# Optimization experiments

Hardware: AMD Instinct MI355X
Metric: run time of the kernel (lower is better)

The kernel has to match this reference:

```python
import jax, jax.numpy as jnp
import numpy as np
import math

EPS = 1e-08
A_CONST = 0.14855178144710912
B_CONST = -0.35487039130661086


def _sdpa(q, k, v):
    # q,k,v: [..., n, d]
    d = q.shape[-1]
    scores = jnp.einsum('...nd,...md->...nm', q / math.sqrt(d), k)
    attn = jax.nn.softmax(scores, axis=-1)
    return jnp.einsum('...nm,...md->...nd', attn, v)


def _lln_attention(q, k, v):
    # global std-based rescaling (torch .std() uses ddof=1), no grad through sigmas
    sig_q = jax.lax.stop_gradient(jnp.std(q, ddof=1))
    sig_k = jax.lax.stop_gradient(jnp.std(k, ddof=1))
    sig_tild = ((sig_q ** 2 * sig_k ** 2 - B_CONST) / (2.0 * A_CONST)) ** 0.5
    alpha = sig_tild / sig_q
    beta = sig_tild / sig_k
    q = alpha * q
    k = beta * k
    q = q - jnp.max(q, axis=-1, keepdims=True)
    k = k - jnp.max(k, axis=(-2, -1), keepdims=True)
    Q = jnp.exp(q)  # [B,H,N,D]
    K = jnp.exp(k)
    # non-causal (mask=None) path
    S = jnp.einsum('bhnd,bhd->bhn', Q, K.sum(axis=-2)) + EPS
    KV = jnp.einsum('bhnd,bhne->bhde', K, v)  # [B,H,D,D]
    out = jnp.einsum('bhnd,bhde->bhne', Q, KV) / S[..., None]
    return out


def _block_diag_attention(q, k, v):
    B, H, N, D = q.shape
    ND = D * (N // D)
    h = H * (ND // D)
    Qb = q[:, :, :ND, :].reshape(B, h, D, D)
    Kb = k[:, :, :ND, :].reshape(B, h, D, D)
    Vb = v[:, :, :ND, :].reshape(B, h, D, D)
    out_blocks = _sdpa(Qb, Kb, Vb).reshape(B, H, ND, D)
    if ND < N:
        out_rem = _sdpa(q[:, :, ND:, :], k[:, :, ND:, :], v[:, :, ND:, :])
        return jnp.concatenate([out_blocks, out_rem], axis=-2)
    return out_blocks


def setup_inputs() -> dict:
    key = jax.random.key(0)
    kq, kk, kv = jax.random.split(key, 3)
    shape = (4, 16, 4096, 64)
    return {
        'q': jax.random.normal(kq, shape, dtype=jnp.float32),
        'k': jax.random.normal(kk, shape, dtype=jnp.float32),
        'v': jax.random.normal(kv, shape, dtype=jnp.float32),
    }


def reference(q, k, v):
    lin = _lln_attention(q, k, v)
    diag = _block_diag_attention(q, k, v)
    return 0.5 * (lin + diag)
```

## Files before the change

### kernel.cpp

```cpp
#include <hip/hip_runtime.h>
#include <math.h>

#define SEQ    4096
#define DIM    64
#define NHEADS 64
#define ELEMS  (NHEADS * SEQ * DIM)

typedef __attribute__((ext_vector_type(8))) short short8;
typedef __attribute__((ext_vector_type(4))) float f32x4;

#define MFMA16(a, b, c) __builtin_amdgcn_mfma_f32_16x16x32_bf16((a), (b), (c), 0, 0, 0)

__device__ __forceinline__ short f2b(float f) {
    union { float f; unsigned u; } x; x.f = f;
    return (short)((x.u + 0x7FFFu + ((x.u >> 16) & 1u)) >> 16);
}

__global__ __launch_bounds__(256) void reduce_stats(const float* __restrict__ q,
                                                    const float* __restrict__ kk,
                                                    float* __restrict__ ws) {
    int bid = blockIdx.x;
    int t = threadIdx.x;
    int isk = bid >> 10;
    int b = bid & 1023;
    const float4* x4 = (const float4*)((isk ? kk : q) + (long)b * 16384);
    float s = 0.f, sq = 0.f, mx = -1e30f;
#pragma unroll
    for (int it = 0; it < 16; ++it) {
        float4 v = x4[it * 256 + t];
        s += v.x + v.y + v.z + v.w;
        sq += v.x * v.x + v.y * v.y + v.z * v.z + v.w * v.w;
        mx = fmaxf(mx, fmaxf(fmaxf(v.x, v.y), fmaxf(v.z, v.w)));
    }
#pragma unroll
    for (int m = 32; m > 0; m >>= 1) {
        s += __shfl_xor(s, m);
        sq += __shfl_xor(sq, m);
        mx = fmaxf(mx, __shfl_xor(mx, m));
    }
    __shared__ float ls[4], lsq[4], lm[4];
    int w = t >> 6, lane = t & 63;
    if (lane == 0) { ls[w] = s; lsq[w] = sq; lm[w] = mx; }
    __syncthreads();
    if (t == 0) {
        float S = 0.f, SQ = 0.f, M = -1e30f;
        for (int i = 0; i < 4; ++i) { S += ls[i]; SQ += lsq[i]; M = fmaxf(M, lm[i]); }
        ws[isk * 2048 + b] = S;
        ws[isk * 2048 + 1024 + b] = SQ;
        if (isk) ws[4096 + b] = M;
    }
}

__global__ __launch_bounds__(256) void compute_params(float* __restrict__ ws) {
    const float* pqs = ws;
    const float* pqq = ws + 1024;
    const float* pks = ws + 2048;
    const float* pkq = ws + 3072;
    const float* pkm = ws + 4096;
    float* params = ws + 5120;
    int t = threadIdx.x;
    float qs = 0.f, qq = 0.f, ks = 0.f, kq = 0.f;
    for (int i = t; i < 1024; i += 256) {
        qs += pqs[i]; qq += pqq[i]; ks += pks[i]; kq += pkq[i];
    }
#pragma unroll
    for (int m = 32; m > 0; m >>= 1) {
        qs += __shfl_xor(qs, m); qq += __shfl_xor(qq, m);
        ks += __shfl_xor(ks, m); kq += __shfl_xor(kq, m);
    }
    __shared__ float l[4][4];
    __shared__ float lab[2];
    int w = t >> 6, lane = t & 63;
    if (lane == 0) { l[w][0] = qs; l[w][1] = qq; l[w][2] = ks; l[w][3] = kq; }
    __syncthreads();
    if (t == 0) {
        float QS = 0.f, QQ = 0.f, KS = 0.f, KQ = 0.f;
        for (int i = 0; i < 4; ++i) { QS += l[i][0]; QQ += l[i][1]; KS += l[i][2]; KQ += l[i][3]; }
        const double M = (double)ELEMS;
        double varq = ((double)QQ - (double)QS * (double)QS / M) / (M - 1.0);
        double vark = ((double)KQ - (double)KS * (double)KS / M) / (M - 1.0);
        const double A = 0.14855178144710912;
        const double B = -0.35487039130661086;
        double st2 = (varq * vark - B) / (2.0 * A);
        float alpha = (float)sqrt(st2 / varq);
        float beta  = (float)sqrt(st2 / vark);
        params[0] = alpha; params[1] = beta;
        lab[0] = alpha; lab[1] = beta;
    }
    __syncthreads();
    if (t < 64) {
        float m = -1e30f;
        for (int i = 0; i < 16; ++i) m = fmaxf(m, pkm[t * 16 + i]);
        params[2 + t] = lab[1] * m;
    }
}

__global__ __launch_bounds__(256, 4) void kv_kernel(const float* __restrict__ k,
                                                    const float* __restrict__ v,
                                                    const float* __restrict__ params,
                                                    float* __restrict__ Ksum,
                                                    float* __restrict__ KVt) {
    __shared__ short kt[64][40];
    __shared__ short vt[64][40];
    int t = threadIdx.x;
    int head = blockIdx.x >> 4, part = blockIdx.x & 15;
    float beta = params[1], kms = params[2 + head];
    int rp = t & 15, cg = t >> 4;
    int w = t >> 6, lane = t & 63;
    int am = lane & 15, ak8 = (lane >> 4) * 8;
    long rowbase = (long)head * SEQ + part * 256;
    f32x4 acc[4];
#pragma unroll
    for (int i = 0; i < 4; ++i) acc[i] = (f32x4)0.f;
    float ksc[4] = {0.f, 0.f, 0.f, 0.f};
    for (int ch = 0; ch < 8; ++ch) {
        long r0 = rowbase + ch * 32 + rp * 2;
        const float* kp = k + r0 * DIM + cg * 4;
        const float* vp = v + r0 * DIM + cg * 4;
        float4 ka = *(const float4*)kp;
        float4 kb2 = *(const float4*)(kp + DIM);
        float4 va = *(const float4*)vp;
        float4 vb2 = *(const float4*)(vp + DIM);
        float ea[4] = {__expf(beta * ka.x - kms), __expf(beta * ka.y - kms),
                       __expf(beta * ka.z - kms), __expf(beta * ka.w - kms)};
        float eb[4] = {__expf(beta * kb2.x - kms), __expf(beta * kb2.y - kms),
                       __expf(beta * kb2.z - kms), __expf(beta * kb2.w - kms)};
        float va_[4] = {va.x, va.y, va.z, va.w};
        float vb_[4] = {vb2.x, vb2.y, vb2.z, vb2.w};
        if (ch) __syncthreads();
#pragma unroll
        for (int j = 0; j < 4; ++j) {
            ksc[j] += ea[j] + eb[j];
            unsigned pk = (unsigned)(unsigned short)f2b(ea[j]) |
                          ((unsigned)(unsigned short)f2b(eb[j]) << 16);
            *(unsigned*)&kt[cg * 4 + j][rp * 2] = pk;
            unsigned pv = (unsigned)(unsigned short)f2b(va_[j]) |
                          ((unsigned)(unsigned short)f2b(vb_[j]) << 16);
            *(unsigned*)&vt[cg * 4 + j][rp * 2] = pv;
        }
        __syncthreads();
        short8 af = *(const short8*)&kt[w * 16 + am][ak8];
#pragma unroll
        for (int nt = 0; nt < 4; ++nt) {
            short8 bf = *(const short8*)&vt[nt * 16 + am][ak8];
            acc[nt] = MFMA16(af, bf, acc[nt]);
        }
    }
    float* KVh = KVt + head * 4096;
#pragma unroll
    for (int nt = 0; nt < 4; ++nt)
#pragma unroll
        for (int r = 0; r < 4; ++r) {
            int d = w * 16 + (lane >> 4) * 4 + r;
            int e = nt * 16 + am;
            atomicAdd(&KVh[e * 64 + d], acc[nt][r]);
        }
#pragma unroll
    for (int m = 1; m < 16; m <<= 1)
#pragma unroll
        for (int j = 0; j < 4; ++j) ksc[j] += __shfl_xor(ksc[j], m);
    if (rp == 0) {
#pragma unroll
        for (int j = 0; j < 4; ++j) atomicAdd(&Ksum[head * 64 + cg * 4 + j], ksc[j]);
    }
}

__global__ __launch_bounds__(256, 4) void fused_kernel(const float* __restrict__ q,
                                                       const float* __restrict__ k,
                                                       const float* __restrict__ v,
                                                       const float* __restrict__ params,
                                                       const float* __restrict__ Ksum,
                                                       const float* __restrict__ KVt,
                                                       float* __restrict__ out) {
    constexpr int LD = 72;
    __shared__ short qb[64][LD];
    __shared__ short kb[64][LD];
    __shared__ short vtb[64][LD];
    __shared__ short kvb[64][LD];
    __shared__ float lksum[64];
    __shared__ float lqmax[64];
    __shared__ float lsinv[64];

    int t = threadIdx.x;
    int head = blockIdx.x >> 6, rb = blockIdx.x & 63;
    long base = ((long)head * SEQ + rb * 64) * DIM;
    float alpha = params[0];
    int w = t >> 6, lane = t & 63;
    int am = lane & 15, ak8 = (lane >> 4) * 8;

    float4 qraw[4];
#pragma unroll
    for (int it = 0; it < 4; ++it) {
        int idx = it * 256 + t;
        int r = idx >> 4, c4 = idx & 15;
        float4 qv = *(const float4*)(q + base + r * DIM + c4 * 4);
        float4 kv2 = *(const float4*)(k + base + r * DIM + c4 * 4);
        float4 kvv = *(const float4*)(KVt + head * 4096 + r * DIM + c4 * 4);
        qraw[it] = qv;
        *(unsigned*)&qb[r][c4 * 4] = (unsigned)(unsigned short)f2b(qv.x) | ((unsigned)(unsigned short)f2b(qv.y) << 16);
        *(unsigned*)&qb[r][c4 * 4 + 2] = (unsigned)(unsigned short)f2b(qv.z) | ((unsigned)(unsigned short)f2b(qv.w) << 16);
        *(unsigned*)&kb[r][c4 * 4] = (unsigned)(unsigned short)f2b(kv2.x) | ((unsigned)(unsigned short)f2b(kv2.y) << 16);
        *(unsigned*)&kb[r][c4 * 4 + 2] = (unsigned)(unsigned short)f2b(kv2.z) | ((unsigned)(unsigned short)f2b(kv2.w) << 16);
        *(unsigned*)&kvb[r][c4 * 4] = (unsigned)(unsigned short)f2b(kvv.x) | ((unsigned)(unsigned short)f2b(kvv.y) << 16);
        *(unsigned*)&kvb[r][c4 * 4 + 2] = (unsigned)(unsigned short)f2b(kvv.z) | ((unsigned)(unsigned short)f2b(kvv.w) << 16);
        float m = fmaxf(fmaxf(qv.x, qv.y), fmaxf(qv.z, qv.w));
#pragma unroll
        for (int msk = 8; msk >= 1; msk >>= 1) m = fmaxf(m, __shfl_xor(m, msk));
        if (c4 == 0) lqmax[r] = m;
    }
#pragma unroll
    for (int it2 = 0; it2 < 2; ++it2) {
        int u = it2 * 256 + t;
        int rp = u & 31, cg = u >> 5;
        const float* vp = v + base + (rp * 2) * DIM + cg * 4;
        float4 va = *(const float4*)vp;
        float4 vb2 = *(const float4*)(vp + DIM);
        float va_[4] = {va.x, va.y, va.z, va.w};
        float vb_[4] = {vb2.x, vb2.y, vb2.z, vb2.w};
#pragma unroll
        for (int j = 0; j < 4; ++j) {
            unsigned pv = (unsigned)(unsigned short)f2b(va_[j]) |
                          ((unsigned)(unsigned short)f2b(vb_[j]) << 16);
            *(unsigned*)&vtb[cg * 4 + j][rp * 2] = pv;
        }
    }
    if (t < 16) *(float4*)&lksum[t * 4] = *(const float4*)(Ksum + head * DIM + t * 4);
    __syncthreads();

    short8 a0 = *(const short8*)&qb[w * 16 + am][ak8];
    short8 a1 = *(const short8*)&qb[w * 16 + am][32 + ak8];
    f32x4 sc[4];
#pragma unroll
    for (int i = 0; i < 4; ++i) sc[i] = (f32x4)0.f;
#pragma unroll
    for (int nt = 0; nt < 4; ++nt) {
        short8 b0 = *(const short8*)&kb[nt * 16 + am][ak8];
        short8 b1 = *(const short8*)&kb[nt * 16 + am][32 + ak8];
        sc[nt] = MFMA16(a0, b0, sc[nt]);
        sc[nt] = MFMA16(a1, b1, sc[nt]);
    }
#pragma unroll
    for (int r = 0; r < 4; ++r) {
        float m = -1e30f;
#pragma unroll
        for (int nt = 0; nt < 4; ++nt) { sc[nt][r] *= 0.125f; m = fmaxf(m, sc[nt][r]); }
#pragma unroll
        for (int msk = 8; msk >= 1; msk >>= 1) m = fmaxf(m, __shfl_xor(m, msk));
        float sum = 0.f;
#pragma unroll
        for (int nt = 0; nt < 4; ++nt) { float e = __expf(sc[nt][r] - m); sc[nt][r] = e; sum += e; }
#pragma unroll
        for (int msk = 8; msk >= 1; msk >>= 1) sum += __shfl_xor(sum, msk);
        float inv = 1.f / sum;
#pragma unroll
        for (int nt = 0; nt < 4; ++nt) sc[nt][r] *= inv;
    }
    unsigned qe[4][2];
#pragma unroll
    for (int it = 0; it < 4; ++it) {
        int idx = it * 256 + t;
        int r = idx >> 4, c4 = idx & 15;
        float am_ = alpha * lqmax[r];
        float e0 = __expf(alpha * qraw[it].x - am_);
        float e1 = __expf(alpha * qraw[it].y - am_);
        float e2 = __expf(alpha * qraw[it].z - am_);
        float e3 = __expf(alpha * qraw[it].w - am_);
        float4 ks4 = *(const float4*)&lksum[c4 * 4];
        float dot = e0 * ks4.x + e1 * ks4.y + e2 * ks4.z + e3 * ks4.w;
#pragma unroll
        for (int msk = 8; msk >= 1; msk >>= 1) dot += __shfl_xor(dot, msk);
        if (c4 == 0) lsinv[r] = 1.f / (dot + 1e-8f);
        qe[it][0] = (unsigned)(unsigned short)f2b(e0) | ((unsigned)(unsigned short)f2b(e1) << 16);
        qe[it][1] = (unsigned)(unsigned short)f2b(e2) | ((unsigned)(unsigned short)f2b(e3) << 16);
    }
    __syncthreads();
#pragma unroll
    for (int it = 0; it < 4; ++it) {
        int idx = it * 256 + t;
        int r = idx >> 4, c4 = idx & 15;
        *(unsigned*)&qb[r][c4 * 4] = qe[it][0];
        *(unsigned*)&qb[r][c4 * 4 + 2] = qe[it][1];
    }
#pragma unroll
    for (int nt = 0; nt < 4; ++nt)
#pragma unroll
        for (int r = 0; r < 4; ++r)
            kb[w * 16 + (lane >> 4) * 4 + r][nt * 16 + am] = f2b(sc[nt][r]);
    __syncthreads();

    short8 pa0 = *(const short8*)&kb[w * 16 + am][ak8];
    short8 pa1 = *(const short8*)&kb[w * 16 + am][32 + ak8];
    short8 qa0 = *(const short8*)&qb[w * 16 + am][ak8];
    short8 qa1 = *(const short8*)&qb[w * 16 + am][32 + ak8];
    f32x4 o[4], acc[4];
#pragma unroll
    for (int i = 0; i < 4; ++i) { o[i] = (f32x4)0.f; acc[i] = (f32x4)0.f; }
#pragma unroll
    for (int nt = 0; nt < 4; ++nt) {
        short8 vb0 = *(const short8*)&vtb[nt * 16 + am][ak8];
        short8 vb1 = *(const short8*)&vtb[nt * 16 + am][32 + ak8];
        o[nt] = MFMA16(pa0, vb0, o[nt]);
        o[nt] = MFMA16(pa1, vb1, o[nt]);
        short8 kb0 = *(const short8*)&kvb[nt * 16 + am][ak8];
        short8 kb1 = *(const short8*)&kvb[nt * 16 + am][32 + ak8];
        acc[nt] = MFMA16(qa0, kb0, acc[nt]);
        acc[nt] = MFMA16(qa1, kb1, acc[nt]);
    }
#pragma unroll
    for (int r = 0; r < 4; ++r) {
        int row = w * 16 + (lane >> 4) * 4 + r;
        float si = lsinv[row];
#pragma unroll
        for (int nt = 0; nt < 4; ++nt)
            out[base + (long)row * DIM + nt * 16 + am] = 0.5f * (acc[nt][r] * si + o[nt][r]);
    }
}

extern "C" void kernel_launch(void* const* d_in, const int* in_sizes, int n_in,
                              void* d_out, int out_size, void* d_ws, size_t ws_size,
                              hipStream_t stream) {
    const float* q = (const float*)d_in[0];
    const float* k = (const float*)d_in[1];
    const float* v = (const float*)d_in[2];
    float* out = (float*)d_out;
    float* ws = (float*)d_ws;
    float* params = ws + 5120;
    float* Ksum = ws + 6144;
    float* KVt = ws + 10240;

    hipMemsetAsync((void*)(ws + 6144), 0, (4096 + 262144) * sizeof(float), stream);

    reduce_stats<<<2048, 256, 0, stream>>>(q, k, ws);
    compute_params<<<1, 256, 0, stream>>>(ws);
    kv_kernel<<<1024, 256, 0, stream>>>(k, v, params, Ksum, KVt);
    fused_kernel<<<4096, 256, 0, stream>>>(q, k, v, params, Ksum, KVt, out);
}
```

Baseline: 322.0 us.

## Replace atomic KV accumulation with partial buffers plus reduction kernel, rework transposes

The KV kernel now uses 512-thread blocks that each cover 512 rows, with double-buffered shared tiles and register prefetch of the next chunk. Each block writes its partial KV and Ksum to a workspace slot instead of doing global atomics, and a new kv_reduce kernel sums the eight partials. This also removes the memset. The fused kernel's V transpose and P store layout are changed to use wider shared-memory stores with a new padding. The cost is an extra launch and roughly 8 MB more workspace traffic.

```diff
diff --git a/kernel.cpp b/kernel.cpp
--- a/kernel.cpp
+++ b/kernel.cpp
@@ -7,6 +7,7 @@
 #define ELEMS  (NHEADS * SEQ * DIM)
 
 typedef __attribute__((ext_vector_type(8))) short short8;
+typedef __attribute__((ext_vector_type(4))) short short4v;
 typedef __attribute__((ext_vector_type(4))) float f32x4;
 
 #define MFMA16(a, b, c) __builtin_amdgcn_mfma_f32_16x16x32_bf16((a), (b), (c), 0, 0, 0)
@@ -15,6 +16,7 @@
     union { float f; unsigned u; } x; x.f = f;
     return (short)((x.u + 0x7FFFu + ((x.u >> 16) & 1u)) >> 16);
 }
+
 
 __global__ __launch_bounds__(256) void reduce_stats(const float* __restrict__ q,
                                                     const float* __restrict__ kk,
@@ -95,73 +97,124 @@
     }
 }
 
-__global__ __launch_bounds__(256, 4) void kv_kernel(const float* __restrict__ k,
+__global__ __launch_bounds__(512, 4) void kv_kernel(const float* __restrict__ k,
                                                     const float* __restrict__ v,
                                                     const float* __restrict__ params,
-                                                    float* __restrict__ Ksum,
-                                                    float* __restrict__ KVt) {
-    __shared__ short kt[64][40];
-    __shared__ short vt[64][40];
+                                                    float* __restrict__ kvpart,
+                                                    float* __restrict__ kspart) {
+    constexpr int LDK = 132;
+    __shared__ short kt[2][64][LDK];
+    __shared__ short vt[2][64][LDK];
+    __shared__ float lksum[64];
     int t = threadIdx.x;
-    int head = blockIdx.x >> 4, part = blockIdx.x & 15;
+    int head = blockIdx.x >> 3, part = blockIdx.x & 7;
     float beta = params[1], kms = params[2 + head];
-    int rp = t & 15, cg = t >> 4;
+    int n0 = t >> 4, m = t & 15;
+    if (t < 64) lksum[t] = 0.f;
+    const float* kb_ = k + ((long)head * SEQ + part * 512) * DIM + m * 4;
+    const float* vb_ = v + ((long)head * SEQ + part * 512) * DIM + m * 4;
+
     int w = t >> 6, lane = t & 63;
-    int am = lane & 15, ak8 = (lane >> 4) * 8;
-    long rowbase = (long)head * SEQ + part * 256;
-    f32x4 acc[4];
-#pragma unroll
-    for (int i = 0; i < 4; ++i) acc[i] = (f32x4)0.f;
+    int dblk = w >> 1, epair = w & 1;
+    int am = lane & 15, q = lane >> 4;
+
+    float kra[4][4], vra[4][4];
+#pragma unroll
+    for (int i = 0; i < 4; ++i) {
+        long off = (long)(n0 + 32 * i) * DIM;
+        float4 x = *(const float4*)(kb_ + off);
+        float4 y = *(const float4*)(vb_ + off);
+        kra[i][0] = x.x; kra[i][1] = x.y; kra[i][2] = x.z; kra[i][3] = x.w;
+        vra[i][0] = y.x; vra[i][1] = y.y; vra[i][2] = y.z; vra[i][3] = y.w;
+    }
+
+    f32x4 acc[2];
+    acc[0] = (f32x4)0.f; acc[1] = (f32x4)0.f;
     float ksc[4] = {0.f, 0.f, 0.f, 0.f};
-    for (int ch = 0; ch < 8; ++ch) {
-        long r0 = rowbase + ch * 32 + rp * 2;
-        const float* kp = k + r0 * DIM + cg * 4;
-        const float* vp = v + r0 * DIM + cg * 4;
-        float4 ka = *(const float4*)kp;
-        float4 kb2 = *(const float4*)(kp + DIM);
-        float4 va = *(const float4*)vp;
-        float4 vb2 = *(const float4*)(vp + DIM);
-        float ea[4] = {__expf(beta * ka.x - kms), __expf(beta * ka.y - kms),
-                       __expf(beta * ka.z - kms), __expf(beta * ka.w - kms)};
-        float eb[4] = {__expf(beta * kb2.x - kms), __expf(beta * kb2.y - kms),
-                       __expf(beta * kb2.z - kms), __expf(beta * kb2.w - kms)};
-        float va_[4] = {va.x, va.y, va.z, va.w};
-        float vb_[4] = {vb2.x, vb2.y, vb2.z, vb2.w};
-        if (ch) __syncthreads();
+
+    for (int c = 0; c < 4; ++c) {
+        int buf = c & 1;
+        float ek[4][4];
+#pragma unroll
+        for (int i = 0; i < 4; ++i)
+#pragma unroll
+            for (int j = 0; j < 4; ++j) {
+                float e = __expf(beta * kra[i][j] - kms);
+                ek[i][j] = e;
+                ksc[j] += e;
+            }
 #pragma unroll
         for (int j = 0; j < 4; ++j) {
-            ksc[j] += ea[j] + eb[j];
-            unsigned pk = (unsigned)(unsigned short)f2b(ea[j]) |
-                          ((unsigned)(unsigned short)f2b(eb[j]) << 16);
-            *(unsigned*)&kt[cg * 4 + j][rp * 2] = pk;
-            unsigned pv = (unsigned)(unsigned short)f2b(va_[j]) |
-                          ((unsigned)(unsigned short)f2b(vb_[j]) << 16);
-            *(unsigned*)&vt[cg * 4 + j][rp * 2] = pv;
+            short4v pk = {f2b(ek[0][j]), f2b(ek[1][j]), f2b(ek[2][j]), f2b(ek[3][j])};
+            short4v pv = {f2b(vra[0][j]), f2b(vra[1][j]), f2b(vra[2][j]), f2b(vra[3][j])};
+            *(short4v*)&kt[buf][4 * m + j][4 * n0] = pk;
+            *(short4v*)&vt[buf][4 * m + j][4 * n0] = pv;
+        }
+        if (c < 3) {
+#pragma unroll
+            for (int i = 0; i < 4; ++i) {
+                long off = (long)((c + 1) * 128 + n0 + 32 * i) * DIM;
+                float4 x = *(const float4*)(kb_ + off);
+                float4 y = *(const float4*)(vb_ + off);
+                kra[i][0] = x.x; kra[i][1] = x.y; kra[i][2] = x.z; kra[i][3] = x.w;
+                vra[i][0] = y.x; vra[i][1] = y.y; vra[i][2] = y.z; vra[i][3] = y.w;
+            }
         }
         __syncthreads();
-        short8 af = *(const short8*)&kt[w * 16 + am][ak8];
-#pragma unroll
-        for (int nt = 0; nt < 4; ++nt) {
-            short8 bf = *(const short8*)&vt[nt * 16 + am][ak8];
-            acc[nt] = MFMA16(af, bf, acc[nt]);
-        }
-    }
-    float* KVh = KVt + head * 4096;
-#pragma unroll
-    for (int nt = 0; nt < 4; ++nt)
-#pragma unroll
-        for (int r = 0; r < 4; ++r) {
-            int d = w * 16 + (lane >> 4) * 4 + r;
-            int e = nt * 16 + am;
-            atomicAdd(&KVh[e * 64 + d], acc[nt][r]);
-        }
-#pragma unroll
-    for (int m = 1; m < 16; m <<= 1)
-#pragma unroll
-        for (int j = 0; j < 4; ++j) ksc[j] += __shfl_xor(ksc[j], m);
-    if (rp == 0) {
-#pragma unroll
-        for (int j = 0; j < 4; ++j) atomicAdd(&Ksum[head * 64 + cg * 4 + j], ksc[j]);
+#pragma unroll
+        for (int ks = 0; ks < 4; ++ks) {
+            int k0 = ks * 32 + q * 8;
+            short4v a0 = *(const short4v*)&kt[buf][dblk * 16 + am][k0];
+            short4v a1 = *(const short4v*)&kt[buf][dblk * 16 + am][k0 + 4];
+            short8 af = __builtin_shufflevector(a0, a1, 0, 1, 2, 3, 4, 5, 6, 7);
+#pragma unroll
+            for (int et = 0; et < 2; ++et) {
+                int e = (epair * 2 + et) * 16 + am;
+                short4v b0 = *(const short4v*)&vt[buf][e][k0];
+                short4v b1 = *(const short4v*)&vt[buf][e][k0 + 4];
+                short8 bf = __builtin_shufflevector(b0, b1, 0, 1, 2, 3, 4, 5, 6, 7);
+                acc[et] = MFMA16(af, bf, acc[et]);
+            }
+        }
+    }
+#pragma unroll
+    for (int j = 0; j < 4; ++j) {
+        ksc[j] += __shfl_xor(ksc[j], 16);
+        ksc[j] += __shfl_xor(ksc[j], 32);
+    }
+    if (q == 0) {
+#pragma unroll
+        for (int j = 0; j < 4; ++j) atomicAdd(&lksum[4 * m + j], ksc[j]);
+    }
+    float* kvp = kvpart + ((long)part * 64 + head) * 4096;
+#pragma unroll
+    for (int et = 0; et < 2; ++et) {
+        int e = (epair * 2 + et) * 16 + am;
+        float4 st;
+        st.x = acc[et][0]; st.y = acc[et][1]; st.z = acc[et][2]; st.w = acc[et][3];
+        *(float4*)&kvp[e * 64 + dblk * 16 + q * 4] = st;
+    }
+    __syncthreads();
+    if (t < 64) kspart[((long)part * 64 + head) * 64 + t] = lksum[t];
+}
+
+__global__ __launch_bounds__(256) void kv_reduce(const float* __restrict__ kvp,
+                                                 const float* __restrict__ ksp,
+                                                 float* __restrict__ KVt,
+                                                 float* __restrict__ Ksum) {
+    int b = blockIdx.x;
+    int idx = b * 256 + threadIdx.x;
+    if (b < 1024) {
+        float s = 0.f;
+#pragma unroll
+        for (int p = 0; p < 8; ++p) s += kvp[p * 262144 + idx];
+        KVt[idx] = s;
+    } else {
+        int i2 = idx - 262144;
+        float s = 0.f;
+#pragma unroll
+        for (int p = 0; p < 8; ++p) s += ksp[p * 4096 + i2];
+        Ksum[i2] = s;
     }
 }
 
@@ -173,10 +226,11 @@
                                                        const float* __restrict__ KVt,
                                                        float* __restrict__ out) {
     constexpr int LD = 72;
+    constexpr int LDV = 68;
     __shared__ short qb[64][LD];
     __shared__ short kb[64][LD];
-    __shared__ short vtb[64][LD];
     __shared__ short kvb[64][LD];
+    __shared__ short vtb[64][LDV];
     __shared__ float lksum[64];
     __shared__ float lqmax[64];
     __shared__ float lsinv[64];
@@ -186,7 +240,7 @@
     long base = ((long)head * SEQ + rb * 64) * DIM;
     float alpha = params[0];
     int w = t >> 6, lane = t & 63;
-    int am = lane & 15, ak8 = (lane >> 4) * 8;
+    int am = lane & 15, q16 = lane >> 4, ak8 = q16 * 8;
 
     float4 qraw[4];
 #pragma unroll
@@ -197,31 +251,29 @@
         float4 kv2 = *(const float4*)(k + base + r * DIM + c4 * 4);
         float4 kvv = *(const float4*)(KVt + head * 4096 + r * DIM + c4 * 4);
         qraw[it] = qv;
-        *(unsigned*)&qb[r][c4 * 4] = (unsigned)(unsigned short)f2b(qv.x) | ((unsigned)(unsigned short)f2b(qv.y) << 16);
+        *(unsigned*)&qb[r][c4 * 4]     = (unsigned)(unsigned short)f2b(qv.x) | ((unsigned)(unsigned short)f2b(qv.y) << 16);
         *(unsigned*)&qb[r][c4 * 4 + 2] = (unsigned)(unsigned short)f2b(qv.z) | ((unsigned)(unsigned short)f2b(qv.w) << 16);
-        *(unsigned*)&kb[r][c4 * 4] = (unsigned)(unsigned short)f2b(kv2.x) | ((unsigned)(unsigned short)f2b(kv2.y) << 16);
+        *(unsigned*)&kb[r][c4 * 4]     = (unsigned)(unsigned short)f2b(kv2.x) | ((unsigned)(unsigned short)f2b(kv2.y) << 16);
         *(unsigned*)&kb[r][c4 * 4 + 2] = (unsigned)(unsigned short)f2b(kv2.z) | ((unsigned)(unsigned short)f2b(kv2.w) << 16);
-        *(unsigned*)&kvb[r][c4 * 4] = (unsigned)(unsigned short)f2b(kvv.x) | ((unsigned)(unsigned short)f2b(kvv.y) << 16);
+        *(unsigned*)&kvb[r][c4 * 4]     = (unsigned)(unsigned short)f2b(kvv.x) | ((unsigned)(unsigned short)f2b(kvv.y) << 16);
         *(unsigned*)&kvb[r][c4 * 4 + 2] = (unsigned)(unsigned short)f2b(kvv.z) | ((unsigned)(unsigned short)f2b(kvv.w) << 16);
-        float m = fmaxf(fmaxf(qv.x, qv.y), fmaxf(qv.z, qv.w));
-#pragma unroll
-        for (int msk = 8; msk >= 1; msk >>= 1) m = fmaxf(m, __shfl_xor(m, msk));
-        if (c4 == 0) lqmax[r] = m;
-    }
-#pragma unroll
-    for (int it2 = 0; it2 < 2; ++it2) {
-        int u = it2 * 256 + t;
-        int rp = u & 31, cg = u >> 5;
-        const float* vp = v + base + (rp * 2) * DIM + cg * 4;
-        float4 va = *(const float4*)vp;
-        float4 vb2 = *(const float4*)(vp + DIM);
-        float va_[4] = {va.x, va.y, va.z, va.w};
-        float vb_[4] = {vb2.x, vb2.y, vb2.z, vb2.w};
+        float mq = fmaxf(fmaxf(qv.x, qv.y), fmaxf(qv.z, qv.w));
+#pragma unroll
+        for (int msk = 8; msk >= 1; msk >>= 1) mq = fmaxf(mq, __shfl_xor(mq, msk));
+        if (c4 == 0) lqmax[r] = mq;
+    }
+    {
+        float vva[4][4];
+#pragma unroll
+        for (int i = 0; i < 4; ++i) {
+            int n = (t >> 4) + 16 * i;
+            float4 x = *(const float4*)(v + base + (long)n * DIM + (t & 15) * 4);
+            vva[i][0] = x.x; vva[i][1] = x.y; vva[i][2] = x.z; vva[i][3] = x.w;
+        }
 #pragma unroll
         for (int j = 0; j < 4; ++j) {
-            unsigned pv = (unsigned)(unsigned short)f2b(va_[j]) |
-                          ((unsigned)(unsigned short)f2b(vb_[j]) << 16);
-            *(unsigned*)&vtb[cg * 4 + j][rp * 2] = pv;
+            short4v pv = {f2b(vva[0][j]), f2b(vva[1][j]), f2b(vva[2][j]), f2b(vva[3][j])};
+            *(short4v*)&vtb[(t & 15) * 4 + j][4 * (t >> 4)] = pv;
         }
     }
     if (t < 16) *(float4*)&lksum[t * 4] = *(const float4*)(Ksum + head * DIM + t * 4);
@@ -241,14 +293,14 @@
     }
 #pragma unroll
     for (int r = 0; r < 4; ++r) {
-        float m = -1e30f;
-#pragma unroll
-        for (int nt = 0; nt < 4; ++nt) { sc[nt][r] *= 0.125f; m = fmaxf(m, sc[nt][r]); }
-#pragma unroll
-        for (int msk = 8; msk >= 1; msk >>= 1) m = fmaxf(m, __shfl_xor(m, msk));
+        float mm = -1e30f;
+#pragma unroll
+        for (int nt = 0; nt < 4; ++nt) { sc[nt][r] *= 0.125f; mm = fmaxf(mm, sc[nt][r]); }
+#pragma unroll
+        for (int msk = 8; msk >= 1; msk >>= 1) mm = fmaxf(mm, __shfl_xor(mm, msk));
         float sum = 0.f;
 #pragma unroll
-        for (int nt = 0; nt < 4; ++nt) { float e = __expf(sc[nt][r] - m); sc[nt][r] = e; sum += e; }
+        for (int nt = 0; nt < 4; ++nt) { float e = __expf(sc[nt][r] - mm); sc[nt][r] = e; sum += e; }
 #pragma unroll
         for (int msk = 8; msk >= 1; msk >>= 1) sum += __shfl_xor(sum, msk);
         float inv = 1.f / sum;
@@ -285,7 +337,7 @@
     for (int nt = 0; nt < 4; ++nt)
 #pragma unroll
         for (int r = 0; r < 4; ++r)
-            kb[w * 16 + (lane >> 4) * 4 + r][nt * 16 + am] = f2b(sc[nt][r]);
+            kb[w * 16 + q16 * 4 + r][4 * am + nt] = f2b(sc[nt][r]);
     __syncthreads();
 
     short8 pa0 = *(const short8*)&kb[w * 16 + am][ak8];
@@ -297,8 +349,12 @@
     for (int i = 0; i < 4; ++i) { o[i] = (f32x4)0.f; acc[i] = (f32x4)0.f; }
 #pragma unroll
     for (int nt = 0; nt < 4; ++nt) {
-        short8 vb0 = *(const short8*)&vtb[nt * 16 + am][ak8];
-        short8 vb1 = *(const short8*)&vtb[nt * 16 + am][32 + ak8];
+        short4v v0a = *(const short4v*)&vtb[nt * 16 + am][ak8];
+        short4v v0b = *(const short4v*)&vtb[nt * 16 + am][ak8 + 4];
+        short4v v1a = *(const short4v*)&vtb[nt * 16 + am][32 + ak8];
+        short4v v1b = *(const short4v*)&vtb[nt * 16 + am][32 + ak8 + 4];
+        short8 vb0 = __builtin_shufflevector(v0a, v0b, 0, 1, 2, 3, 4, 5, 6, 7);
+        short8 vb1 = __builtin_shufflevector(v1a, v1b, 0, 1, 2, 3, 4, 5, 6, 7);
         o[nt] = MFMA16(pa0, vb0, o[nt]);
         o[nt] = MFMA16(pa1, vb1, o[nt]);
         short8 kb0 = *(const short8*)&kvb[nt * 16 + am][ak8];
@@ -308,7 +364,7 @@
     }
 #pragma unroll
     for (int r = 0; r < 4; ++r) {
-        int row = w * 16 + (lane >> 4) * 4 + r;
+        int row = w * 16 + q16 * 4 + r;
         float si = lsinv[row];
 #pragma unroll
         for (int nt = 0; nt < 4; ++nt)
@@ -325,13 +381,14 @@
     float* out = (float*)d_out;
     float* ws = (float*)d_ws;
     float* params = ws + 5120;
-    float* Ksum = ws + 6144;
-    float* KVt = ws + 10240;
-
-    hipMemsetAsync((void*)(ws + 6144), 0, (4096 + 262144) * sizeof(float), stream);
+    float* KVt    = ws + 8192;
+    float* Ksum   = ws + 270336;
+    float* kvpart = ws + 274432;
+    float* kspart = ws + 2371584;
 
     reduce_stats<<<2048, 256, 0, stream>>>(q, k, ws);
     compute_params<<<1, 256, 0, stream>>>(ws);
-    kv_kernel<<<1024, 256, 0, stream>>>(k, v, params, Ksum, KVt);
+    kv_kernel<<<512, 512, 0, stream>>>(k, v, params, kvpart, kspart);
+    kv_reduce<<<1040, 256, 0, stream>>>(kvpart, kspart, KVt, Ksum);
     fused_kernel<<<4096, 256, 0, stream>>>(q, k, v, params, Ksum, KVt, out);
 }
```

Result: faster. 267.5 us (-16.9%).
